# Kernel optimization log

Measured on AMD Instinct MI355X. Metric: run time of the kernel, lower is better.

## Reference

```python
import jax, jax.numpy as jnp
import numpy as np

DIM, DEPTH, DH, CH, SH = 512, 2, 64, 2, 8
B, T, N = 8, 1024, 2048
CI, SI, FF = CH * DH, SH * DH, 4 * DIM


def layer_norm(x, w, b, eps=1e-5):
    m = jnp.mean(x, -1, keepdims=True)
    v = jnp.var(x, -1, keepdims=True)
    return (x - m) * jax.lax.rsqrt(v + eps) * w + b


def rotate_half(x):
    # interleaved pairs: (x0,x1) -> (-x1,x0)
    x1, x2 = x[..., 0::2], x[..., 1::2]
    return jnp.stack((-x2, x1), axis=-1).reshape(x.shape)


def apply_rot(freqs, x):
    return x * jnp.cos(freqs) + rotate_half(x) * jnp.sin(freqs)


def split_heads(x, h):
    b, t, _ = x.shape
    return x.reshape(b, t, h, -1).transpose(0, 2, 1, 3)


def merge_heads(x):
    b, h, t, d = x.shape
    return x.transpose(0, 2, 1, 3).reshape(b, t, h * d)


def rotary_attn(q, k, v, q_pos, k_pos, heads, mask=None):
    # q:(B,Tq,H*Dh), k/v:(B,Tk,H*Dh), pos:(B,T,Dh); rotate_value=False -> v untouched
    qh, kh, vh = split_heads(q, heads), split_heads(k, heads), split_heads(v, heads)
    qh = apply_rot(q_pos[:, None], qh)
    kh = apply_rot(k_pos[:, None], kh)
    scores = jnp.einsum('bhqd,bhkd->bhqk', qh, kh) * (DH ** -0.5)
    if mask is not None:
        scores = jnp.where(mask, scores, jnp.finfo(scores.dtype).min)
    attn = jax.nn.softmax(scores, axis=-1)
    return merge_heads(jnp.einsum('bhqk,bhkd->bhqd', attn, vh))


def _forward(bin_queries, bin_time_emb, encoder_latents, latent_time_emb,
             ca_lnq_w, ca_lnq_b, ca_lnc_w, ca_lnc_b, ca_wq, ca_wkv, ca_wo, ca_bo,
             sa_ln_w, sa_ln_b, sa_wqkv, sa_wo, sa_bo,
             ffn_ln_w, ffn_ln_b, ffn_w1, ffn_b1, ffn_w2, ffn_b2):
    Tq = bin_queries.shape[1]
    mask = jnp.tril(jnp.ones((Tq, Tq), dtype=bool))[None, None]  # (1,1,T,T) causal
    x = bin_queries
    for l in range(DEPTH):
        # 1) rotary cross-attention to history latents
        xn = layer_norm(x, ca_lnq_w[l], ca_lnq_b[l])
        cn = layer_norm(encoder_latents, ca_lnc_w[l], ca_lnc_b[l])
        q = xn @ ca_wq[l]
        k, v = jnp.split(cn @ ca_wkv[l], 2, axis=-1)
        x = x + rotary_attn(q, k, v, bin_time_emb, latent_time_emb, CH) @ ca_wo[l] + ca_bo[l]
        # 2) causal rotary self-attention over bin queries
        xn = layer_norm(x, sa_ln_w[l], sa_ln_b[l])
        q, k, v = jnp.split(xn @ sa_wqkv[l], 3, axis=-1)
        x = x + rotary_attn(q, k, v, bin_time_emb, bin_time_emb, SH, mask) @ sa_wo[l] + sa_bo[l]
        # 3) pre-LN FFN with GEGLU (mult=4), dropout off in eval
        h = layer_norm(x, ffn_ln_w[l], ffn_ln_b[l])
        a, g = jnp.split(h @ ffn_w1[l] + ffn_b1[l], 2, axis=-1)
        x = x + (a * jax.nn.gelu(g, approximate=False)) @ ffn_w2[l] + ffn_b2[l]
    return x


def setup_inputs() -> dict:
    key = jax.random.key(0)
    ks = jax.random.split(key, 12)
    n = lambda i, shape, s: jax.random.normal(ks[i], shape, dtype=jnp.float32) * s
    return {
        'bin_queries': n(0, (B, T, DIM), 1.0),
        'bin_time_emb': n(1, (B, T, DH), 1.0),
        'encoder_latents': n(2, (B, N, DIM), 1.0),
        'latent_time_emb': n(3, (B, N, DH), 1.0),
        'ca_lnq_w': jnp.ones((DEPTH, DIM)), 'ca_lnq_b': jnp.zeros((DEPTH, DIM)),
        'ca_lnc_w': jnp.ones((DEPTH, DIM)), 'ca_lnc_b': jnp.zeros((DEPTH, DIM)),
        'ca_wq': n(4, (DEPTH, DIM, CI), 0.02), 'ca_wkv': n(5, (DEPTH, DIM, 2 * CI), 0.02),
        'ca_wo': n(6, (DEPTH, CI, DIM), 0.02), 'ca_bo': jnp.zeros((DEPTH, DIM)),
        'sa_ln_w': jnp.ones((DEPTH, DIM)), 'sa_ln_b': jnp.zeros((DEPTH, DIM)),
        'sa_wqkv': n(7, (DEPTH, DIM, 3 * SI), 0.02), 'sa_wo': n(8, (DEPTH, SI, DIM), 0.02),
        'sa_bo': jnp.zeros((DEPTH, DIM)),
        'ffn_ln_w': jnp.ones((DEPTH, DIM)), 'ffn_ln_b': jnp.zeros((DEPTH, DIM)),
        'ffn_w1': n(9, (DEPTH, DIM, 2 * FF), 0.02), 'ffn_b1': jnp.zeros((DEPTH, 2 * FF)),
        'ffn_w2': n(10, (DEPTH, FF, DIM), 0.02), 'ffn_b2': jnp.zeros((DEPTH, DIM)),
    }


def reference(bin_queries, bin_time_emb, encoder_latents, latent_time_emb,
              ca_lnq_w, ca_lnq_b, ca_lnc_w, ca_lnc_b, ca_wq, ca_wkv, ca_wo, ca_bo,
              sa_ln_w, sa_ln_b, sa_wqkv, sa_wo, sa_bo,
              ffn_ln_w, ffn_ln_b, ffn_w1, ffn_b1, ffn_w2, ffn_b2):
    return _forward(bin_queries, bin_time_emb, encoder_latents, latent_time_emb,
                    ca_lnq_w, ca_lnq_b, ca_lnc_w, ca_lnc_b, ca_wq, ca_wkv, ca_wo, ca_bo,
                    sa_ln_w, sa_ln_b, sa_wqkv, sa_wo, sa_bo,
                    ffn_ln_w, ffn_ln_b, ffn_w1, ffn_b1, ffn_w2, ffn_b2)
```

## Files before the change

### kernel.cpp

```cpp
#include <hip/hip_runtime.h>
#include <cstdint>
#include <cstddef>

static constexpr int DIMc = 512;
static constexpr int DHc  = 64;
static constexpr int CHc  = 2;
static constexpr int SHc  = 8;
static constexpr int Bc   = 8;
static constexpr int Tc   = 1024;
static constexpr int Nc   = 2048;
static constexpr int CIc  = CHc * DHc;
static constexpr int SIc  = SHc * DHc;
static constexpr int FFc  = 4 * DIMc;
static constexpr int RQ   = Bc * Tc;
static constexpr int RL   = Bc * Nc;

typedef short bf16x8 __attribute__((ext_vector_type(8)));
typedef float f32x4  __attribute__((ext_vector_type(4)));

__device__ __forceinline__ ushort f2bf(float f) {
  uint32_t u = __builtin_bit_cast(uint32_t, f);
  u += 0x7fffu + ((u >> 16) & 1u);
  return (ushort)(u >> 16);
}
__device__ __forceinline__ uint32_t packbf2(float a, float b) {
  return (uint32_t)f2bf(a) | ((uint32_t)f2bf(b) << 16);
}
__device__ __forceinline__ float bf2f(ushort h) {
  uint32_t u = ((uint32_t)h) << 16;
  return __builtin_bit_cast(float, u);
}

__device__ __forceinline__ void gload_lds16(const ushort* g, ushort* lds) {
  __builtin_amdgcn_global_load_lds(
      (const __attribute__((address_space(1))) void*)g,
      (__attribute__((address_space(3))) void*)lds, 16, 0, 0);
}

__device__ __forceinline__ float gelu_fast(float g) {
  float u = g * (0.7978845608f + 0.0356774081f * g * g);
  float e = __expf(2.f * u);
  float th = 1.f - 2.f * __builtin_amdgcn_rcpf(1.f + e);
  return 0.5f * g * (1.f + th);
}

__device__ __forceinline__ float rope_rot(int odd, float v, float p, float2 cs) {
  return odd ? (v * cs.x + p * cs.y) : (v * cs.x - p * cs.y);
}

__global__ __launch_bounds__(256) void trig_prep(const float* __restrict__ src,
    float2* __restrict__ dst, int n) {
  int i = blockIdx.x * 256 + threadIdx.x;
  if (i >= n) return;
  float s, c;
  __sincosf(src[i], &s, &c);
  dst[i] = make_float2(c, s);
}

__global__ __launch_bounds__(256) void ln_rows(const float* __restrict__ X,
    const float* __restrict__ w, const float* __restrict__ b,
    ushort* __restrict__ out, int rows) {
  int gw = (int)((blockIdx.x * 256 + threadIdx.x) >> 6);
  int lane = threadIdx.x & 63;
  if (gw >= rows) return;
  const float* xr = X + (size_t)gw * DIMc;
  float4 v0 = *(const float4*)(xr + lane * 8);
  float4 v1 = *(const float4*)(xr + lane * 8 + 4);
  float xv[8] = {v0.x, v0.y, v0.z, v0.w, v1.x, v1.y, v1.z, v1.w};
  float s = 0.f, ss = 0.f;
#pragma unroll
  for (int i = 0; i < 8; i++) { s += xv[i]; ss += xv[i] * xv[i]; }
#pragma unroll
  for (int off = 32; off; off >>= 1) { s += __shfl_xor(s, off); ss += __shfl_xor(ss, off); }
  float mean = s * (1.f / DIMc);
  float var = ss * (1.f / DIMc) - mean * mean;
  float r = rsqrtf(var + 1e-5f);
  int c = lane * 8;
  ushort o[8] __attribute__((aligned(16)));
#pragma unroll
  for (int i = 0; i < 8; i++) o[i] = f2bf((xv[i] - mean) * r * w[c + i] + b[c + i]);
  *(uint4*)(out + (size_t)gw * DIMc + c) = *(const uint4*)o;
}

__global__ __launch_bounds__(256) void wtrans_all(
    const float* __restrict__ wq, const float* __restrict__ wkv,
    const float* __restrict__ wo, const float* __restrict__ qkv,
    const float* __restrict__ swo, const float* __restrict__ w1,
    const float* __restrict__ w2, ushort* __restrict__ dst, int layer) {
  constexpr int Ks[7]   = {512, 512, 128, 512, 512, 512, 2048};
  constexpr int Ns[7]   = {128, 256, 512, 1536, 512, 4096, 512};
  constexpr int pre[8]  = {0, 64, 192, 256, 1024, 1280, 3328, 4352};
  constexpr int dOff[7] = {0, 65536, 196608, 262144, 1048576, 1310720, 3407872};
  int bid = blockIdx.x;
  int wid = 0;
#pragma unroll
  for (int i = 1; i < 7; i++) wid += (bid >= pre[i]);
  int tileIdx = bid - pre[wid];
  int K = Ks[wid], N = Ns[wid];
  const float* srcs[7] = {wq, wkv, wo, qkv, swo, w1, w2};
  const float* W = srcs[wid] + (size_t)layer * K * N;
  ushort* Wt = dst + dOff[wid];
  int ntx = N / 32;
  int n0 = (tileIdx % ntx) * 32, k0 = (tileIdx / ntx) * 32;
  __shared__ float tile[32][33];
  int tx = threadIdx.x & 31, ty = threadIdx.x >> 5;
#pragma unroll
  for (int i = 0; i < 32; i += 8)
    tile[ty + i][tx] = W[(size_t)(k0 + ty + i) * N + n0 + tx];
  __syncthreads();
  if (wid == 5) {
#pragma unroll
    for (int i = 0; i < 32; i += 8) {
      int nrow = n0 + ty + i;
      int p = nrow & 2047;
      int rowT = ((p >> 4) << 5) + ((nrow < 2048) ? 0 : 16) + (p & 15);
      Wt[(size_t)rowT * K + k0 + tx] = f2bf(tile[tx][ty + i]);
    }
  } else {
#pragma unroll
    for (int i = 0; i < 32; i += 8)
      Wt[(size_t)(n0 + ty + i) * K + k0 + tx] = f2bf(tile[tx][ty + i]);
  }
}

template<int MODE>
__global__ __launch_bounds__(256) void gemm128(const ushort* __restrict__ A,
    const ushort* __restrict__ Bt, const float* __restrict__ bias,
    const float* __restrict__ resIn, float* __restrict__ resOut,
    ushort* __restrict__ outB, int M, int N, int K,
    const float2* __restrict__ cs, ushort* __restrict__ vt) {
  __shared__ __align__(16) ushort As[128 * 64];
  __shared__ __align__(16) ushort Bs[128 * 64];
  int t = threadIdx.x, wv = t >> 6, lane = t & 63;
  int bm = blockIdx.y, bn = blockIdx.x;
  int fr = lane & 15, g = lane >> 4;
  int wr = (wv >> 1) * 64, wc = (wv & 1) * 64;
  int srow = wv * 32 + (lane >> 3);
  int sslot = lane & 7;
  const ushort* Abase = A + (size_t)(bm * 128) * K;
  const ushort* Bbase = Bt + (size_t)(bn * 128) * K;

  f32x4 acc[4][4] = {};
  for (int k0 = 0; k0 < K; k0 += 64) {
#pragma unroll
    for (int j = 0; j < 4; j++) {
      int r = srow + j * 8;
      int kc = sslot ^ (r & 7);
      gload_lds16(Abase + (size_t)r * K + k0 + kc * 8, As + (wv * 256 + j * 64) * 8);
      gload_lds16(Bbase + (size_t)r * K + k0 + kc * 8, Bs + (wv * 256 + j * 64) * 8);
    }
    __syncthreads();
#pragma unroll
    for (int ks = 0; ks < 2; ks++) {
      bf16x8 af[4], bf[4];
#pragma unroll
      for (int mm = 0; mm < 4; mm++) {
        int row = wr + mm * 16 + fr;
        af[mm] = *(const bf16x8*)(As + row * 64 + (((ks * 4 + g) ^ (row & 7)) * 8));
      }
#pragma unroll
      for (int nn = 0; nn < 4; nn++) {
        int row = wc + nn * 16 + fr;
        bf[nn] = *(const bf16x8*)(Bs + row * 64 + (((ks * 4 + g) ^ (row & 7)) * 8));
      }
#pragma unroll
      for (int mm = 0; mm < 4; mm++)
#pragma unroll
        for (int nn = 0; nn < 4; nn++)
          acc[mm][nn] = __builtin_amdgcn_mfma_f32_16x16x32_bf16(af[mm], bf[nn], acc[mm][nn], 0, 0, 0);
    }
    __syncthreads();
  }

  if (MODE == 2) {
    int NH = N >> 1;
#pragma unroll
    for (int mm = 0; mm < 4; mm++)
#pragma unroll
      for (int np = 0; np < 2; np++) {
        int ocol = bn * 64 + (wc >> 1) + np * 16 + fr;
        float ba = bias[ocol];
        float bg = bias[NH + ocol];
#pragma unroll
        for (int i = 0; i < 4; i++) {
          int gr = bm * 128 + wr + mm * 16 + g * 4 + i;
          float a = acc[mm][np * 2][i] + ba;
          float gv = acc[mm][np * 2 + 1][i] + bg;
          outB[(size_t)gr * NH + ocol] = f2bf(a * gelu_fast(gv));
        }
      }
  } else if (MODE == 3) {
    if (bn * 128 < 1024) {
#pragma unroll
      for (int mm = 0; mm < 4; mm++)
#pragma unroll
        for (int nn = 0; nn < 4; nn++) {
          int gc = bn * 128 + wc + nn * 16 + fr;
          int d = gc & 63;
          float sc = (gc < 512) ? 0.125f : 1.f;
#pragma unroll
          for (int i = 0; i < 4; i++) {
            int gr = bm * 128 + wr + mm * 16 + g * 4 + i;
            float val = acc[mm][nn][i];
            float prt = __shfl_xor(val, 1);
            float2 csv = cs[(size_t)gr * 64 + d];
            outB[(size_t)gr * N + gc] = f2bf(rope_rot(fr & 1, val, prt, csv) * sc);
          }
        }
    } else {
#pragma unroll
      for (int mm = 0; mm < 4; mm++)
#pragma unroll
        for (int nn = 0; nn < 4; nn++) {
          int gc = bn * 128 + wc + nn * 16 + fr;
          int ch = gc - 1024;
          int gr0 = bm * 128 + wr + mm * 16 + g * 4;
          int bb = gr0 >> 10, t0 = gr0 & 1023;
          uint2 w;
          w.x = packbf2(acc[mm][nn][0], acc[mm][nn][1]);
          w.y = packbf2(acc[mm][nn][2], acc[mm][nn][3]);
          *(uint2*)(vt + ((size_t)bb * 512 + ch) * 1024 + t0) = w;
        }
    }
  } else {
#pragma unroll
    for (int mm = 0; mm < 4; mm++)
#pragma unroll
      for (int nn = 0; nn < 4; nn++)
#pragma unroll
        for (int i = 0; i < 4; i++) {
          int gr = bm * 128 + wr + mm * 16 + g * 4 + i;
          int gc = bn * 128 + wc + nn * 16 + fr;
          float val = acc[mm][nn][i] + (bias ? bias[gc] : 0.f);
          if (MODE == 0) outB[(size_t)gr * N + gc] = f2bf(val);
          else resOut[(size_t)gr * N + gc] = resIn[(size_t)gr * N + gc] + val;
        }
  }
}

template<int MODE>
__global__ __launch_bounds__(256) void gemm128x64(const ushort* __restrict__ A,
    const ushort* __restrict__ Bt, const float* __restrict__ bias,
    const float* __restrict__ resIn, float* __restrict__ resOut,
    ushort* __restrict__ outB, int M, int N, int K,
    const float2* __restrict__ cs, ushort* __restrict__ vt) {
  __shared__ __align__(16) ushort As[128 * 64];
  __shared__ __align__(16) ushort Bs[64 * 64];
  int t = threadIdx.x, wv = t >> 6, lane = t & 63;
  int bm = blockIdx.y, bn = blockIdx.x;
  int fr = lane & 15, g = lane >> 4;
  int wr = (wv >> 1) * 64, wc = (wv & 1) * 32;
  const ushort* Abase = A + (size_t)(bm * 128) * K;
  const ushort* Bbase = Bt + (size_t)(bn * 64) * K;

  f32x4 acc[4][2] = {};
  for (int k0 = 0; k0 < K; k0 += 64) {
#pragma unroll
    for (int j = 0; j < 4; j++) {
      int c = j * 256 + wv * 64 + lane;
      int r = c >> 3, s = c & 7;
      int kc = s ^ (r & 7);
      gload_lds16(Abase + (size_t)r * K + k0 + kc * 8, As + (j * 256 + wv * 64) * 8);
      if (j < 2)
        gload_lds16(Bbase + (size_t)r * K + k0 + kc * 8, Bs + (j * 256 + wv * 64) * 8);
    }
    __syncthreads();
#pragma unroll
    for (int ks = 0; ks < 2; ks++) {
      bf16x8 af[4], bf[2];
#pragma unroll
      for (int mm = 0; mm < 4; mm++) {
        int row = wr + mm * 16 + fr;
        af[mm] = *(const bf16x8*)(As + row * 64 + (((ks * 4 + g) ^ (row & 7)) * 8));
      }
#pragma unroll
      for (int nn = 0; nn < 2; nn++) {
        int row = wc + nn * 16 + fr;
        bf[nn] = *(const bf16x8*)(Bs + row * 64 + (((ks * 4 + g) ^ (row & 7)) * 8));
      }
#pragma unroll
      for (int mm = 0; mm < 4; mm++)
#pragma unroll
        for (int nn = 0; nn < 2; nn++)
          acc[mm][nn] = __builtin_amdgcn_mfma_f32_16x16x32_bf16(af[mm], bf[nn], acc[mm][nn], 0, 0, 0);
    }
    __syncthreads();
  }

  if (MODE == 3) {
    if (bn * 64 < 128) {
#pragma unroll
      for (int mm = 0; mm < 4; mm++)
#pragma unroll
        for (int nn = 0; nn < 2; nn++) {
          int gc = bn * 64 + wc + nn * 16 + fr;
          int d = gc & 63;
#pragma unroll
          for (int i = 0; i < 4; i++) {
            int gr = bm * 128 + wr + mm * 16 + g * 4 + i;
            float val = acc[mm][nn][i];
            float prt = __shfl_xor(val, 1);
            float2 csv = cs[(size_t)gr * 64 + d];
            outB[(size_t)gr * N + gc] = f2bf(rope_rot(fr & 1, val, prt, csv));
          }
        }
    } else {
#pragma unroll
      for (int mm = 0; mm < 4; mm++)
#pragma unroll
        for (int nn = 0; nn < 2; nn++) {
          int gc = bn * 64 + wc + nn * 16 + fr;
          int ch = gc - 128;
          int gr0 = bm * 128 + wr + mm * 16 + g * 4;
          int bb = gr0 >> 11, t0 = gr0 & 2047;
          uint2 w;
          w.x = packbf2(acc[mm][nn][0], acc[mm][nn][1]);
          w.y = packbf2(acc[mm][nn][2], acc[mm][nn][3]);
          *(uint2*)(vt + ((size_t)bb * 128 + ch) * 2048 + t0) = w;
        }
    }
  } else {
#pragma unroll
    for (int mm = 0; mm < 4; mm++)
#pragma unroll
      for (int nn = 0; nn < 2; nn++)
#pragma unroll
        for (int i = 0; i < 4; i++) {
          int gr = bm * 128 + wr + mm * 16 + g * 4 + i;
          int gc = bn * 64 + wc + nn * 16 + fr;
          float val = acc[mm][nn][i] + (bias ? bias[gc] : 0.f);
          if (MODE == 0) outB[(size_t)gr * N + gc] = f2bf(val);
          else resOut[(size_t)gr * N + gc] = resIn[(size_t)gr * N + gc] + val;
        }
  }
}

__global__ __launch_bounds__(256) void gemm64_rope(const ushort* __restrict__ A,
    const ushort* __restrict__ Bt, ushort* __restrict__ outB,
    const float2* __restrict__ cs, int M, int N, int K) {
  __shared__ __align__(16) ushort As[64][40];
  __shared__ __align__(16) ushort Bs[64][40];
  int t = threadIdx.x;
  int bm = blockIdx.y, bn = blockIdx.x;
  int row = t >> 2, kc = (t & 3) << 3;
  const ushort* aG = A + (size_t)(bm * 64 + row) * K + kc;
  const ushort* bG = Bt + (size_t)(bn * 64 + row) * K + kc;
  int wv = t >> 6, lane = t & 63;
  int wr = (wv >> 1) * 32, wc = (wv & 1) * 32;
  int fr = lane & 15, fk = (lane >> 4) << 3;
  f32x4 acc[2][2] = {};
  for (int k0 = 0; k0 < K; k0 += 32) {
    *(uint4*)&As[row][kc] = *(const uint4*)(aG + k0);
    *(uint4*)&Bs[row][kc] = *(const uint4*)(bG + k0);
    __syncthreads();
    bf16x8 a0 = *(const bf16x8*)&As[wr + fr][fk];
    bf16x8 a1 = *(const bf16x8*)&As[wr + 16 + fr][fk];
    bf16x8 b0 = *(const bf16x8*)&Bs[wc + fr][fk];
    bf16x8 b1 = *(const bf16x8*)&Bs[wc + 16 + fr][fk];
    acc[0][0] = __builtin_amdgcn_mfma_f32_16x16x32_bf16(a0, b0, acc[0][0], 0, 0, 0);
    acc[0][1] = __builtin_amdgcn_mfma_f32_16x16x32_bf16(a0, b1, acc[0][1], 0, 0, 0);
    acc[1][0] = __builtin_amdgcn_mfma_f32_16x16x32_bf16(a1, b0, acc[1][0], 0, 0, 0);
    acc[1][1] = __builtin_amdgcn_mfma_f32_16x16x32_bf16(a1, b1, acc[1][1], 0, 0, 0);
    __syncthreads();
  }
  int cr0 = wr + ((lane >> 4) << 2);
  int cc0 = wc + fr;
#pragma unroll
  for (int mm = 0; mm < 2; mm++)
#pragma unroll
    for (int nn = 0; nn < 2; nn++) {
      int gc = bn * 64 + cc0 + nn * 16;
      int d = gc & 63;
#pragma unroll
      for (int i = 0; i < 4; i++) {
        int gr = bm * 64 + cr0 + mm * 16 + i;
        float val = acc[mm][nn][i];
        float prt = __shfl_xor(val, 1);
        float2 csv = cs[(size_t)gr * 64 + d];
        outB[(size_t)gr * N + gc] = f2bf(rope_rot(fr & 1, val, prt, csv) * 0.125f);
      }
    }
}

template<int CAUSAL>
__global__ __launch_bounds__(256) void attn_mfma(
    const ushort* __restrict__ Q, const ushort* __restrict__ K,
    const ushort* __restrict__ Vt, ushort* __restrict__ O,
    int qStride, int kStride, int kOff, int oStride,
    int Tq, int NK, int H) {
  __shared__ __align__(16) ushort Ks[64 * 64];
  __shared__ __align__(16) ushort Vs[64 * 64];
  __shared__ __align__(16) ushort Ps[4][16 * 72];
  int b = blockIdx.z, h = blockIdx.y;
  int qt = CAUSAL ? ((int)gridDim.x - 1 - (int)blockIdx.x) : blockIdx.x;
  int t = threadIdx.x, wv = t >> 6, lane = t & 63;
  int g = lane >> 4, fr = lane & 15;
  int qw = qt * 64 + wv * 16;
  int HD = H * 64;

  const ushort* qrow = Q + (size_t)(b * Tq + qw + fr) * qStride + h * 64;
  bf16x8 qlo = *(const bf16x8*)(qrow + g * 8);
  bf16x8 qhi = *(const bf16x8*)(qrow + 32 + g * 8);

  f32x4 o_acc[4] = {};
  float m_run = -1e30f, l_run = 0.f;

  uint32_t* Pw = (uint32_t*)&Ps[wv][0];
  int ntiles = CAUSAL ? (qt + 1) : (NK / 64);
  for (int kt = 0; kt < ntiles; kt++) {
    int k0 = kt * 64;
    __syncthreads();
#pragma unroll
    for (int i = 0; i < 2; i++) {
      int id = t + i * 256;
      int r = id >> 3, c = id & 7;
      uint4 kval = *(const uint4*)(K + (size_t)(b * NK + k0 + r) * kStride + kOff + h * 64 + c * 8);
      *(uint4*)(Ks + r * 64 + ((c ^ (r & 7)) * 8)) = kval;
      uint4 vval = *(const uint4*)(Vt + ((size_t)b * HD + h * 64 + r) * NK + k0 + c * 8);
      *(uint4*)(Vs + r * 64 + ((c ^ (r & 7)) * 8)) = vval;
    }
    __syncthreads();

    f32x4 s[4];
#pragma unroll
    for (int nn = 0; nn < 4; nn++) {
      int row = nn * 16 + fr;
      bf16x8 kf0 = *(const bf16x8*)(Ks + row * 64 + ((g ^ (fr & 7)) * 8));
      bf16x8 kf1 = *(const bf16x8*)(Ks + row * 64 + (((4 + g) ^ (fr & 7)) * 8));
      f32x4 z = {};
      z = __builtin_amdgcn_mfma_f32_16x16x32_bf16(kf0, qlo, z, 0, 0, 0);
      z = __builtin_amdgcn_mfma_f32_16x16x32_bf16(kf1, qhi, z, 0, 0, 0);
      s[nn] = z;
    }
    if (CAUSAL && (k0 + 63 > qw)) {
#pragma unroll
      for (int nn = 0; nn < 4; nn++)
#pragma unroll
        for (int i = 0; i < 4; i++)
          if (k0 + nn * 16 + g * 4 + i > qw + fr) s[nn][i] = -1e30f;
    }
    float tm = s[0][0];
#pragma unroll
    for (int nn = 0; nn < 4; nn++)
#pragma unroll
      for (int i = 0; i < 4; i++) tm = fmaxf(tm, s[nn][i]);
    tm = fmaxf(tm, __shfl_xor(tm, 16));
    tm = fmaxf(tm, __shfl_xor(tm, 32));
    float mnew = fmaxf(m_run, tm);
    float corr = __expf(m_run - mnew);
    float ps = 0.f;
#pragma unroll
    for (int nn = 0; nn < 4; nn++)
#pragma unroll
      for (int i = 0; i < 4; i++) {
        float p = __expf(s[nn][i] - mnew);
        s[nn][i] = p;
        ps += p;
      }
    ps += __shfl_xor(ps, 16);
    ps += __shfl_xor(ps, 32);
    l_run = l_run * corr + ps;
    m_run = mnew;
#pragma unroll
    for (int dd = 0; dd < 4; dd++) o_acc[dd] *= corr;
#pragma unroll
    for (int nn = 0; nn < 4; nn++)
#pragma unroll
      for (int p = 0; p < 2; p++)
        Pw[fr * 36 + 8 * nn + 2 * g + p] = packbf2(s[nn][2 * p], s[nn][2 * p + 1]);
    bf16x8 pa0 = *(const bf16x8*)(&Ps[wv][fr * 72 + g * 8]);
    bf16x8 pa1 = *(const bf16x8*)(&Ps[wv][fr * 72 + 32 + g * 8]);
#pragma unroll
    for (int dd = 0; dd < 4; dd++) {
      int row = dd * 16 + fr;
      bf16x8 vf0 = *(const bf16x8*)(Vs + row * 64 + ((g ^ (fr & 7)) * 8));
      bf16x8 vf1 = *(const bf16x8*)(Vs + row * 64 + (((4 + g) ^ (fr & 7)) * 8));
      o_acc[dd] = __builtin_amdgcn_mfma_f32_16x16x32_bf16(vf0, pa0, o_acc[dd], 0, 0, 0);
      o_acc[dd] = __builtin_amdgcn_mfma_f32_16x16x32_bf16(vf1, pa1, o_acc[dd], 0, 0, 0);
    }
  }
  float rl = 1.f / l_run;
  ushort* obase = O + (size_t)(b * Tq + qw + fr) * oStride + h * 64;
#pragma unroll
  for (int dd = 0; dd < 4; dd++) {
    uint2 w;
    w.x = packbf2(o_acc[dd][0] * rl, o_acc[dd][1] * rl);
    w.y = packbf2(o_acc[dd][2] * rl, o_acc[dd][3] * rl);
    *(uint2*)(obase + dd * 16 + g * 4) = w;
  }
}

extern "C" void kernel_launch(void* const* d_in, const int* in_sizes, int n_in,
                              void* d_out, int out_size, void* d_ws, size_t ws_size,
                              hipStream_t stream) {
  const float* bin_queries = (const float*)d_in[0];
  const float* bin_time    = (const float*)d_in[1];
  const float* latents     = (const float*)d_in[2];
  const float* lat_time    = (const float*)d_in[3];
  const float* ca_lnq_w = (const float*)d_in[4];
  const float* ca_lnq_b = (const float*)d_in[5];
  const float* ca_lnc_w = (const float*)d_in[6];
  const float* ca_lnc_b = (const float*)d_in[7];
  const float* ca_wq  = (const float*)d_in[8];
  const float* ca_wkv = (const float*)d_in[9];
  const float* ca_wo  = (const float*)d_in[10];
  const float* ca_bo  = (const float*)d_in[11];
  const float* sa_ln_w = (const float*)d_in[12];
  const float* sa_ln_b = (const float*)d_in[13];
  const float* sa_wqkv = (const float*)d_in[14];
  const float* sa_wo   = (const float*)d_in[15];
  const float* sa_bo   = (const float*)d_in[16];
  const float* ffn_ln_w = (const float*)d_in[17];
  const float* ffn_ln_b = (const float*)d_in[18];
  const float* ffn_w1 = (const float*)d_in[19];
  const float* ffn_b1 = (const float*)d_in[20];
  const float* ffn_w2 = (const float*)d_in[21];
  const float* ffn_b2 = (const float*)d_in[22];

  constexpr size_t X_BYTES = (size_t)RQ * DIMc * 4;
  char* ws = (char*)d_ws;
  float* x = (float*)ws;
  char* A0 = ws + X_BYTES;
  ushort* cn     = (ushort*)(A0);
  ushort* ca_xn  = (ushort*)(A0 + 16777216);
  ushort* qbuf   = (ushort*)(A0 + 25165824);
  ushort* kv     = (ushort*)(A0 + 27262976);
  ushort* ca_att = (ushort*)(A0 + 35651584);
  ushort* vt_c   = (ushort*)(A0 + 37748736);
  ushort* sa_xn  = (ushort*)(A0);
  ushort* qkv    = (ushort*)(A0 + 8388608);
  ushort* sa_att = (ushort*)(A0 + 33554432);
  ushort* vt_s   = (ushort*)(A0 + 41943040);
  ushort* hb     = (ushort*)(A0);
  ushort* ag     = (ushort*)(A0 + 8388608);
  float2* csQ = (float2*)(A0 + 62914560);
  float2* csL = (float2*)(A0 + 67108864);
  char* W0 = A0 + 109051904;
  ushort* wbase = (ushort*)W0;
  ushort* wqT  = wbase;
  ushort* wkvT = wbase + 65536;
  ushort* woT  = wbase + 196608;
  ushort* qkvT = wbase + 262144;
  ushort* swoT = wbase + 1048576;
  ushort* w1T  = wbase + 1310720;
  ushort* w2T  = wbase + 3407872;

  trig_prep<<<(RQ * 64) / 256, 256, 0, stream>>>(bin_time, csQ, RQ * 64);
  trig_prep<<<(RL * 64) / 256, 256, 0, stream>>>(lat_time, csL, RL * 64);

  for (int l = 0; l < 2; l++) {
    wtrans_all<<<4352, 256, 0, stream>>>(ca_wq, ca_wkv, ca_wo, sa_wqkv, sa_wo,
                                         ffn_w1, ffn_w2, wbase, l);

    const float* xin = (l == 0) ? bin_queries : x;
    ln_rows<<<RQ / 4, 256, 0, stream>>>(xin, ca_lnq_w + l * DIMc, ca_lnq_b + l * DIMc, ca_xn, RQ);
    ln_rows<<<RL / 4, 256, 0, stream>>>(latents, ca_lnc_w + l * DIMc, ca_lnc_b + l * DIMc, cn, RL);
    gemm64_rope<<<dim3(CIc / 64, RQ / 64), 256, 0, stream>>>(ca_xn, wqT, qbuf, csQ, RQ, CIc, DIMc);
    gemm128x64<3><<<dim3(2 * CIc / 64, RL / 128), 256, 0, stream>>>(cn, wkvT, nullptr,
        nullptr, nullptr, kv, RL, 2 * CIc, DIMc, csL, vt_c);
    attn_mfma<0><<<dim3(Tc / 64, CHc, Bc), 256, 0, stream>>>(qbuf, kv, vt_c, ca_att,
        CIc, 2 * CIc, 0, CIc, Tc, Nc, CHc);
    gemm128x64<1><<<dim3(DIMc / 64, RQ / 128), 256, 0, stream>>>(ca_att, woT, ca_bo + l * DIMc,
        xin, x, nullptr, RQ, DIMc, CIc, nullptr, nullptr);

    ln_rows<<<RQ / 4, 256, 0, stream>>>(x, sa_ln_w + l * DIMc, sa_ln_b + l * DIMc, sa_xn, RQ);
    gemm128<3><<<dim3(3 * SIc / 128, RQ / 128), 256, 0, stream>>>(sa_xn, qkvT, nullptr,
        nullptr, nullptr, qkv, RQ, 3 * SIc, DIMc, csQ, vt_s);
    attn_mfma<1><<<dim3(Tc / 64, SHc, Bc), 256, 0, stream>>>(qkv, qkv, vt_s, sa_att,
        3 * SIc, 3 * SIc, SIc, SIc, Tc, Tc, SHc);
    gemm128x64<1><<<dim3(DIMc / 64, RQ / 128), 256, 0, stream>>>(sa_att, swoT, sa_bo + l * DIMc,
        x, x, nullptr, RQ, DIMc, SIc, nullptr, nullptr);

    ln_rows<<<RQ / 4, 256, 0, stream>>>(x, ffn_ln_w + l * DIMc, ffn_ln_b + l * DIMc, hb, RQ);
    gemm128<2><<<dim3(2 * FFc / 128, RQ / 128), 256, 0, stream>>>(hb, w1T,
        ffn_b1 + (size_t)l * 2 * FFc, nullptr, nullptr, ag, RQ, 2 * FFc, DIMc, nullptr, nullptr);
    float* resOut = (l == 1) ? (float*)d_out : x;
    gemm128x64<1><<<dim3(DIMc / 64, RQ / 128), 256, 0, stream>>>(ag, w2T, ffn_b2 + l * DIMc,
        x, resOut, nullptr, RQ, DIMc, FFc, nullptr, nullptr);
  }
}
```

Before: 634.1 us.

## Add 256x256 double-buffered GEMM with fused GEGLU epilogue for FFN up-projection

Replaces the 128x128 FFN first-layer GEMM (with its GEGLU epilogue) with a new 512-thread kernel using 256x256 tiles. It double-buffers LDS through direct global-to-LDS loads, uses an XOR swizzle and inline ds_read_b128, and raises wave priority around the MFMA bursts. Larger tiles raise arithmetic intensity and cut global traffic on the largest GEMM. The cost is 128KB of LDS per block, which lowers occupancy. The epilogue assumes the weight columns are interleaved so that the value and gate columns of each pair land in adjacent fragments.

```diff
diff --git a/kernel.cpp b/kernel.cpp
--- a/kernel.cpp
+++ b/kernel.cpp
@@ -35,6 +35,14 @@
   __builtin_amdgcn_global_load_lds(
       (const __attribute__((address_space(1))) void*)g,
       (__attribute__((address_space(3))) void*)lds, 16, 0, 0);
+}
+
+__device__ __forceinline__ bf16x8 ds_read8(const ushort* p) {
+  bf16x8 d;
+  asm volatile("ds_read_b128 %0, %1"
+               : "=v"(d)
+               : "v"((const __attribute__((address_space(3))) ushort*)p));
+  return d;
 }
 
 __device__ __forceinline__ float gelu_fast(float g) {
@@ -236,6 +244,100 @@
           else resOut[(size_t)gr * N + gc] = resIn[(size_t)gr * N + gc] + val;
         }
   }
+}
+
+__global__ __launch_bounds__(512, 2) void gemm256_gelu(
+    const ushort* __restrict__ A, const ushort* __restrict__ Bt,
+    const float* __restrict__ bias, ushort* __restrict__ outB,
+    int M, int N, int K) {
+  __shared__ __align__(16) ushort As[2][256 * 64];
+  __shared__ __align__(16) ushort Bs[2][256 * 64];
+  int t = threadIdx.x, wv = t >> 6, lane = t & 63;
+  int bm = blockIdx.y, bn = blockIdx.x;
+  int fr = lane & 15, g = lane >> 4;
+  int wr = (wv >> 2) * 128, wc = (wv & 3) * 64;
+  int srow = wv * 32 + (lane >> 3);
+  int sslot = lane & 7;
+  const ushort* Abase = A + (size_t)(bm * 256) * K;
+  const ushort* Bbase = Bt + (size_t)(bn * 256) * K;
+
+  f32x4 acc[8][4] = {};
+  int nt = K >> 6;
+
+#define STG256(buf, kt)                                                       \
+  {                                                                           \
+    _Pragma("unroll")                                                         \
+    for (int j = 0; j < 4; j++) {                                             \
+      int r = srow + j * 8;                                                   \
+      int kc = sslot ^ (r & 7);                                               \
+      gload_lds16(Abase + (size_t)r * K + (kt) * 64 + kc * 8,                 \
+                  &As[buf][(wv * 256 + j * 64) * 8]);                         \
+      gload_lds16(Bbase + (size_t)r * K + (kt) * 64 + kc * 8,                 \
+                  &Bs[buf][(wv * 256 + j * 64) * 8]);                         \
+    }                                                                         \
+  }
+
+  STG256(0, 0);
+  STG256(1, 1);
+
+  for (int tt = 0; tt < nt; tt++) {
+    int cur = tt & 1;
+    if (tt + 1 < nt) asm volatile("s_waitcnt vmcnt(8)" ::: "memory");
+    else             asm volatile("s_waitcnt vmcnt(0)" ::: "memory");
+    __builtin_amdgcn_s_barrier();
+    const ushort* Ac = As[cur];
+    const ushort* Bc = Bs[cur];
+#pragma unroll
+    for (int ph = 0; ph < 4; ph++) {
+      const int mh = ph >> 1, nh = ph & 1;
+      bf16x8 af[2][4], bf[2][2];
+#pragma unroll
+      for (int ks = 0; ks < 2; ks++) {
+#pragma unroll
+        for (int mi = 0; mi < 4; mi++) {
+          int row = wr + (mh * 4 + mi) * 16 + fr;
+          af[ks][mi] = ds_read8(Ac + row * 64 + (((ks * 4 + g) ^ (row & 7)) * 8));
+        }
+#pragma unroll
+        for (int ni = 0; ni < 2; ni++) {
+          int row = wc + (nh * 2 + ni) * 16 + fr;
+          bf[ks][ni] = ds_read8(Bc + row * 64 + (((ks * 4 + g) ^ (row & 7)) * 8));
+        }
+      }
+      asm volatile("s_waitcnt lgkmcnt(0)" ::: "memory");
+      __builtin_amdgcn_sched_barrier(0);
+      __builtin_amdgcn_s_setprio(1);
+#pragma unroll
+      for (int ks = 0; ks < 2; ks++)
+#pragma unroll
+        for (int mi = 0; mi < 4; mi++)
+#pragma unroll
+          for (int ni = 0; ni < 2; ni++)
+            acc[mh * 4 + mi][nh * 2 + ni] = __builtin_amdgcn_mfma_f32_16x16x32_bf16(
+                af[ks][mi], bf[ks][ni], acc[mh * 4 + mi][nh * 2 + ni], 0, 0, 0);
+      __builtin_amdgcn_s_setprio(0);
+      __builtin_amdgcn_s_barrier();
+    }
+    if (tt + 2 < nt) STG256(cur, tt + 2);
+  }
+#undef STG256
+
+  int NH = N >> 1;
+#pragma unroll
+  for (int mf = 0; mf < 8; mf++)
+#pragma unroll
+    for (int np = 0; np < 2; np++) {
+      int ocol = bn * 128 + (wc >> 1) + np * 16 + fr;
+      float ba = bias[ocol];
+      float bg = bias[NH + ocol];
+#pragma unroll
+      for (int i = 0; i < 4; i++) {
+        int gr = bm * 256 + wr + mf * 16 + g * 4 + i;
+        float a = acc[mf][np * 2][i] + ba;
+        float gv = acc[mf][np * 2 + 1][i] + bg;
+        outB[(size_t)gr * NH + ocol] = f2bf(a * gelu_fast(gv));
+      }
+    }
 }
 
 template<int MODE>
@@ -572,8 +674,8 @@
         x, x, nullptr, RQ, DIMc, SIc, nullptr, nullptr);
 
     ln_rows<<<RQ / 4, 256, 0, stream>>>(x, ffn_ln_w + l * DIMc, ffn_ln_b + l * DIMc, hb, RQ);
-    gemm128<2><<<dim3(2 * FFc / 128, RQ / 128), 256, 0, stream>>>(hb, w1T,
-        ffn_b1 + (size_t)l * 2 * FFc, nullptr, nullptr, ag, RQ, 2 * FFc, DIMc, nullptr, nullptr);
+    gemm256_gelu<<<dim3(2 * FFc / 256, RQ / 256), 512, 0, stream>>>(hb, w1T,
+        ffn_b1 + (size_t)l * 2 * FFc, ag, RQ, 2 * FFc, DIMc);
     float* resOut = (l == 1) ? (float*)d_out : x;
     gemm128x64<1><<<dim3(DIMc / 64, RQ / 128), 256, 0, stream>>>(ag, w2T, ffn_b2 + l * DIMc,
         x, resOut, nullptr, RQ, DIMc, FFc, nullptr, nullptr);
```

Result: no change. 628.4 us (-0.9%).

## Split cross-attention KV range across blocks, prefetch KV tiles, hoist latent layernorms

Applied to the files above, without the earlier changes.

Cross-attention is split into two KV halves per head, each writing partial outputs and max/sum stats, then merged by a separate combine kernel. This doubles the grid for the low-head-count cross-attention (2 heads × 16 q-tiles × 8 batches), which otherwise underfills the GPU. Both attention kernels now load the next K/V tile into registers while computing on the current one. The two per-layer latent layernorms are fused into one kernel run before the loop, since they depend only on the inputs. The cost is an extra fp32 partial buffer round trip and one more launch.

```diff
diff --git a/kernel.cpp b/kernel.cpp
--- a/kernel.cpp
+++ b/kernel.cpp
@@ -80,6 +80,34 @@
 #pragma unroll
   for (int i = 0; i < 8; i++) o[i] = f2bf((xv[i] - mean) * r * w[c + i] + b[c + i]);
   *(uint4*)(out + (size_t)gw * DIMc + c) = *(const uint4*)o;
+}
+
+__global__ __launch_bounds__(256) void ln_rows2(const float* __restrict__ X,
+    const float* __restrict__ w, const float* __restrict__ b,
+    ushort* __restrict__ out0, ushort* __restrict__ out1, int rows) {
+  int gw = (int)((blockIdx.x * 256 + threadIdx.x) >> 6);
+  int lane = threadIdx.x & 63;
+  if (gw >= rows) return;
+  const float* xr = X + (size_t)gw * DIMc;
+  float4 v0 = *(const float4*)(xr + lane * 8);
+  float4 v1 = *(const float4*)(xr + lane * 8 + 4);
+  float xv[8] = {v0.x, v0.y, v0.z, v0.w, v1.x, v1.y, v1.z, v1.w};
+  float s = 0.f, ss = 0.f;
+#pragma unroll
+  for (int i = 0; i < 8; i++) { s += xv[i]; ss += xv[i] * xv[i]; }
+#pragma unroll
+  for (int off = 32; off; off >>= 1) { s += __shfl_xor(s, off); ss += __shfl_xor(ss, off); }
+  float mean = s * (1.f / DIMc);
+  float var = ss * (1.f / DIMc) - mean * mean;
+  float r = rsqrtf(var + 1e-5f);
+  int c = lane * 8;
+  ushort o[8] __attribute__((aligned(16)));
+#pragma unroll
+  for (int i = 0; i < 8; i++) o[i] = f2bf((xv[i] - mean) * r * w[c + i] + b[c + i]);
+  *(uint4*)(out0 + (size_t)gw * DIMc + c) = *(const uint4*)o;
+#pragma unroll
+  for (int i = 0; i < 8; i++) o[i] = f2bf((xv[i] - mean) * r * w[DIMc + c + i] + b[DIMc + c + i]);
+  *(uint4*)(out1 + (size_t)gw * DIMc + c) = *(const uint4*)o;
 }
 
 __global__ __launch_bounds__(256) void wtrans_all(
@@ -382,8 +410,28 @@
     }
 }
 
-template<int CAUSAL>
-__global__ __launch_bounds__(256) void attn_mfma(
+#define ATTN_LOAD_REGS(k0)                                                    \
+  {                                                                           \
+    _Pragma("unroll")                                                         \
+    for (int j = 0; j < 2; j++) {                                             \
+      int r = (t >> 3) + j * 32, c = t & 7;                                   \
+      kreg[j] = *(const uint4*)(K + (size_t)(b * NK + (k0) + r) * kStride +   \
+                                kOff + h * 64 + c * 8);                       \
+      vreg[j] = *(const uint4*)(Vt + ((size_t)b * HD + h * 64 + r) * NK +     \
+                                (k0) + c * 8);                                \
+    }                                                                         \
+  }
+#define ATTN_STORE_LDS()                                                      \
+  {                                                                           \
+    _Pragma("unroll")                                                         \
+    for (int j = 0; j < 2; j++) {                                             \
+      int r = (t >> 3) + j * 32, c = t & 7;                                   \
+      *(uint4*)(Ks + r * 64 + ((c ^ (r & 7)) * 8)) = kreg[j];                 \
+      *(uint4*)(Vs + r * 64 + ((c ^ (r & 7)) * 8)) = vreg[j];                 \
+    }                                                                         \
+  }
+
+__global__ __launch_bounds__(256) void attn_causal(
     const ushort* __restrict__ Q, const ushort* __restrict__ K,
     const ushort* __restrict__ Vt, ushort* __restrict__ O,
     int qStride, int kStride, int kOff, int oStride,
@@ -392,7 +440,7 @@
   __shared__ __align__(16) ushort Vs[64 * 64];
   __shared__ __align__(16) ushort Ps[4][16 * 72];
   int b = blockIdx.z, h = blockIdx.y;
-  int qt = CAUSAL ? ((int)gridDim.x - 1 - (int)blockIdx.x) : blockIdx.x;
+  int qt = (int)gridDim.x - 1 - (int)blockIdx.x;
   int t = threadIdx.x, wv = t >> 6, lane = t & 63;
   int g = lane >> 4, fr = lane & 15;
   int qw = qt * 64 + wv * 16;
@@ -404,22 +452,17 @@
 
   f32x4 o_acc[4] = {};
   float m_run = -1e30f, l_run = 0.f;
-
   uint32_t* Pw = (uint32_t*)&Ps[wv][0];
-  int ntiles = CAUSAL ? (qt + 1) : (NK / 64);
+  int ntiles = qt + 1;
+
+  uint4 kreg[2], vreg[2];
+  ATTN_LOAD_REGS(0);
   for (int kt = 0; kt < ntiles; kt++) {
     int k0 = kt * 64;
     __syncthreads();
-#pragma unroll
-    for (int i = 0; i < 2; i++) {
-      int id = t + i * 256;
-      int r = id >> 3, c = id & 7;
-      uint4 kval = *(const uint4*)(K + (size_t)(b * NK + k0 + r) * kStride + kOff + h * 64 + c * 8);
-      *(uint4*)(Ks + r * 64 + ((c ^ (r & 7)) * 8)) = kval;
-      uint4 vval = *(const uint4*)(Vt + ((size_t)b * HD + h * 64 + r) * NK + k0 + c * 8);
-      *(uint4*)(Vs + r * 64 + ((c ^ (r & 7)) * 8)) = vval;
-    }
-    __syncthreads();
+    ATTN_STORE_LDS();
+    __syncthreads();
+    if (kt + 1 < ntiles) ATTN_LOAD_REGS(k0 + 64);
 
     f32x4 s[4];
 #pragma unroll
@@ -432,7 +475,7 @@
       z = __builtin_amdgcn_mfma_f32_16x16x32_bf16(kf1, qhi, z, 0, 0, 0);
       s[nn] = z;
     }
-    if (CAUSAL && (k0 + 63 > qw)) {
+    if (k0 + 63 > qw) {
 #pragma unroll
       for (int nn = 0; nn < 4; nn++)
 #pragma unroll
@@ -488,6 +531,122 @@
     w.y = packbf2(o_acc[dd][2] * rl, o_acc[dd][3] * rl);
     *(uint2*)(obase + dd * 16 + g * 4) = w;
   }
+}
+
+__global__ __launch_bounds__(256) void attn_split(
+    const ushort* __restrict__ Q, const ushort* __restrict__ K,
+    const ushort* __restrict__ Vt, float* __restrict__ Opart,
+    float2* __restrict__ mlpart,
+    int qStride, int kStride, int kOff, int Tq, int NK, int H) {
+  __shared__ __align__(16) ushort Ks[64 * 64];
+  __shared__ __align__(16) ushort Vs[64 * 64];
+  __shared__ __align__(16) ushort Ps[4][16 * 72];
+  int b = blockIdx.z;
+  int h = blockIdx.y >> 1, sp = blockIdx.y & 1;
+  int qt = blockIdx.x;
+  int t = threadIdx.x, wv = t >> 6, lane = t & 63;
+  int g = lane >> 4, fr = lane & 15;
+  int qw = qt * 64 + wv * 16;
+  int HD = H * 64;
+  int half = NK / 128;
+  int ktbeg = sp * half, ktend = ktbeg + half;
+
+  const ushort* qrow = Q + (size_t)(b * Tq + qw + fr) * qStride + h * 64;
+  bf16x8 qlo = *(const bf16x8*)(qrow + g * 8);
+  bf16x8 qhi = *(const bf16x8*)(qrow + 32 + g * 8);
+
+  f32x4 o_acc[4] = {};
+  float m_run = -1e30f, l_run = 0.f;
+  uint32_t* Pw = (uint32_t*)&Ps[wv][0];
+
+  uint4 kreg[2], vreg[2];
+  ATTN_LOAD_REGS(ktbeg * 64);
+  for (int kt = ktbeg; kt < ktend; kt++) {
+    __syncthreads();
+    ATTN_STORE_LDS();
+    __syncthreads();
+    if (kt + 1 < ktend) ATTN_LOAD_REGS((kt + 1) * 64);
+
+    f32x4 s[4];
+#pragma unroll
+    for (int nn = 0; nn < 4; nn++) {
+      int row = nn * 16 + fr;
+      bf16x8 kf0 = *(const bf16x8*)(Ks + row * 64 + ((g ^ (fr & 7)) * 8));
+      bf16x8 kf1 = *(const bf16x8*)(Ks + row * 64 + (((4 + g) ^ (fr & 7)) * 8));
+      f32x4 z = {};
+      z = __builtin_amdgcn_mfma_f32_16x16x32_bf16(kf0, qlo, z, 0, 0, 0);
+      z = __builtin_amdgcn_mfma_f32_16x16x32_bf16(kf1, qhi, z, 0, 0, 0);
+      s[nn] = z;
+    }
+    float tm = s[0][0];
+#pragma unroll
+    for (int nn = 0; nn < 4; nn++)
+#pragma unroll
+      for (int i = 0; i < 4; i++) tm = fmaxf(tm, s[nn][i]);
+    tm = fmaxf(tm, __shfl_xor(tm, 16));
+    tm = fmaxf(tm, __shfl_xor(tm, 32));
+    float mnew = fmaxf(m_run, tm);
+    float corr = __expf(m_run - mnew);
+    float ps = 0.f;
+#pragma unroll
+    for (int nn = 0; nn < 4; nn++)
+#pragma unroll
+      for (int i = 0; i < 4; i++) {
+        float p = __expf(s[nn][i] - mnew);
+        s[nn][i] = p;
+        ps += p;
+      }
+    ps += __shfl_xor(ps, 16);
+    ps += __shfl_xor(ps, 32);
+    l_run = l_run * corr + ps;
+    m_run = mnew;
+#pragma unroll
+    for (int dd = 0; dd < 4; dd++) o_acc[dd] *= corr;
+#pragma unroll
+    for (int nn = 0; nn < 4; nn++)
+#pragma unroll
+      for (int p = 0; p < 2; p++)
+        Pw[fr * 36 + 8 * nn + 2 * g + p] = packbf2(s[nn][2 * p], s[nn][2 * p + 1]);
+    bf16x8 pa0 = *(const bf16x8*)(&Ps[wv][fr * 72 + g * 8]);
+    bf16x8 pa1 = *(const bf16x8*)(&Ps[wv][fr * 72 + 32 + g * 8]);
+#pragma unroll
+    for (int dd = 0; dd < 4; dd++) {
+      int row = dd * 16 + fr;
+      bf16x8 vf0 = *(const bf16x8*)(Vs + row * 64 + ((g ^ (fr & 7)) * 8));
+      bf16x8 vf1 = *(const bf16x8*)(Vs + row * 64 + (((4 + g) ^ (fr & 7)) * 8));
+      o_acc[dd] = __builtin_amdgcn_mfma_f32_16x16x32_bf16(vf0, pa0, o_acc[dd], 0, 0, 0);
+      o_acc[dd] = __builtin_amdgcn_mfma_f32_16x16x32_bf16(vf1, pa1, o_acc[dd], 0, 0, 0);
+    }
+  }
+  size_t pslot = ((size_t)(b * H + h) * 2 + sp) * Tq + qw + fr;
+  float* obase = Opart + pslot * 64;
+#pragma unroll
+  for (int dd = 0; dd < 4; dd++)
+    *(float4*)(obase + dd * 16 + g * 4) = *(float4*)&o_acc[dd];
+  if (g == 0) mlpart[pslot] = make_float2(m_run, l_run);
+}
+
+__global__ __launch_bounds__(256) void attn_combine(
+    const float* __restrict__ Opart, const float2* __restrict__ mlpart,
+    ushort* __restrict__ O, int Tq, int H, int oStride) {
+  int idx = blockIdx.x * 256 + threadIdx.x;
+  int dq = (idx & 15) * 4;
+  int tt = (idx >> 4) & (Tq - 1);
+  int hh = idx >> 14;
+  int b = hh / H, h = hh % H;
+  size_t base0 = (((size_t)hh * 2 + 0) * Tq + tt) * 64 + dq;
+  size_t base1 = base0 + (size_t)Tq * 64;
+  float2 ml0 = mlpart[((size_t)hh * 2 + 0) * Tq + tt];
+  float2 ml1 = mlpart[((size_t)hh * 2 + 1) * Tq + tt];
+  float M = fmaxf(ml0.x, ml1.x);
+  float w0 = __expf(ml0.x - M), w1 = __expf(ml1.x - M);
+  float rl = 1.f / (w0 * ml0.y + w1 * ml1.y);
+  float4 o0 = *(const float4*)(Opart + base0);
+  float4 o1 = *(const float4*)(Opart + base1);
+  uint2 w;
+  w.x = packbf2((w0 * o0.x + w1 * o1.x) * rl, (w0 * o0.y + w1 * o1.y) * rl);
+  w.y = packbf2((w0 * o0.z + w1 * o1.z) * rl, (w0 * o0.w + w1 * o1.w) * rl);
+  *(uint2*)(O + (size_t)(b * Tq + tt) * oStride + h * 64 + dq) = w;
 }
 
 extern "C" void kernel_launch(void* const* d_in, const int* in_sizes, int n_in,
@@ -533,8 +692,11 @@
   ushort* vt_s   = (ushort*)(A0 + 41943040);
   ushort* hb     = (ushort*)(A0);
   ushort* ag     = (ushort*)(A0 + 8388608);
-  float2* csQ = (float2*)(A0 + 62914560);
-  float2* csL = (float2*)(A0 + 67108864);
+  float2* csQ    = (float2*)(A0 + 62914560);
+  float2* csL    = (float2*)(A0 + 67108864);
+  ushort* cn2    = (ushort*)(A0 + 79691776);
+  float*  Opart  = (float*)(A0 + 96468992);
+  float2* mlpart = (float2*)(A0 + 104857600);
   char* W0 = A0 + 109051904;
   ushort* wbase = (ushort*)W0;
   ushort* wqT  = wbase;
@@ -547,26 +709,29 @@
 
   trig_prep<<<(RQ * 64) / 256, 256, 0, stream>>>(bin_time, csQ, RQ * 64);
   trig_prep<<<(RL * 64) / 256, 256, 0, stream>>>(lat_time, csL, RL * 64);
+  ln_rows2<<<RL / 4, 256, 0, stream>>>(latents, ca_lnc_w, ca_lnc_b, cn, cn2, RL);
 
   for (int l = 0; l < 2; l++) {
     wtrans_all<<<4352, 256, 0, stream>>>(ca_wq, ca_wkv, ca_wo, sa_wqkv, sa_wo,
                                          ffn_w1, ffn_w2, wbase, l);
 
     const float* xin = (l == 0) ? bin_queries : x;
+    const ushort* cnl = (l == 0) ? cn : cn2;
     ln_rows<<<RQ / 4, 256, 0, stream>>>(xin, ca_lnq_w + l * DIMc, ca_lnq_b + l * DIMc, ca_xn, RQ);
-    ln_rows<<<RL / 4, 256, 0, stream>>>(latents, ca_lnc_w + l * DIMc, ca_lnc_b + l * DIMc, cn, RL);
     gemm64_rope<<<dim3(CIc / 64, RQ / 64), 256, 0, stream>>>(ca_xn, wqT, qbuf, csQ, RQ, CIc, DIMc);
-    gemm128x64<3><<<dim3(2 * CIc / 64, RL / 128), 256, 0, stream>>>(cn, wkvT, nullptr,
+    gemm128x64<3><<<dim3(2 * CIc / 64, RL / 128), 256, 0, stream>>>(cnl, wkvT, nullptr,
         nullptr, nullptr, kv, RL, 2 * CIc, DIMc, csL, vt_c);
-    attn_mfma<0><<<dim3(Tc / 64, CHc, Bc), 256, 0, stream>>>(qbuf, kv, vt_c, ca_att,
-        CIc, 2 * CIc, 0, CIc, Tc, Nc, CHc);
+    attn_split<<<dim3(Tc / 64, CHc * 2, Bc), 256, 0, stream>>>(qbuf, kv, vt_c,
+        Opart, mlpart, CIc, 2 * CIc, 0, Tc, Nc, CHc);
+    attn_combine<<<(Bc * CHc * Tc * 16) / 256, 256, 0, stream>>>(Opart, mlpart,
+        ca_att, Tc, CHc, CIc);
     gemm128x64<1><<<dim3(DIMc / 64, RQ / 128), 256, 0, stream>>>(ca_att, woT, ca_bo + l * DIMc,
         xin, x, nullptr, RQ, DIMc, CIc, nullptr, nullptr);
 
     ln_rows<<<RQ / 4, 256, 0, stream>>>(x, sa_ln_w + l * DIMc, sa_ln_b + l * DIMc, sa_xn, RQ);
     gemm128<3><<<dim3(3 * SIc / 128, RQ / 128), 256, 0, stream>>>(sa_xn, qkvT, nullptr,
         nullptr, nullptr, qkv, RQ, 3 * SIc, DIMc, csQ, vt_s);
-    attn_mfma<1><<<dim3(Tc / 64, SHc, Bc), 256, 0, stream>>>(qkv, qkv, vt_s, sa_att,
+    attn_causal<<<dim3(Tc / 64, SHc, Bc), 256, 0, stream>>>(qkv, qkv, vt_s, sa_att,
         3 * SIc, 3 * SIc, SIc, SIc, Tc, Tc, SHc);
     gemm128x64<1><<<dim3(DIMc / 64, RQ / 128), 256, 0, stream>>>(sa_att, swoT, sa_bo + l * DIMc,
         x, x, nullptr, RQ, DIMc, SIc, nullptr, nullptr);
```

Result: slower. 704.7 us (median of 3 runs) (+11.1%).
